# Performance work log

Hardware: AMD Instinct MI355X
Metric: run time of the kernel (lower is better)

Reference implementation:

```python
import jax, jax.numpy as jnp
import numpy as np

T = 2048          # tokens (flattened batch*seq, vLLM style)
HID = 2048        # hidden_size
NH = 16           # num_heads
D_NOPE = 128
D_ROPE = 64
D_QK = D_NOPE + D_ROPE   # 192
D_V = 128
Q_LORA = 1536
KV_LORA = 512
THETA = 10000.0
EPS = 1e-6
SCALING = D_QK ** -0.5


def _rmsnorm(x, g):
    return x * jax.lax.rsqrt(jnp.mean(x * x, axis=-1, keepdims=True) + EPS) * g


def _rope(pos, x):
    # interleaved (is_neox_style=False) rotary embedding
    d = x.shape[-1]
    inv = 1.0 / (THETA ** (jnp.arange(0, d, 2, dtype=jnp.float32) / d))
    f = pos.astype(jnp.float32)[:, None] * inv          # [T, d/2]
    cos, sin = jnp.cos(f), jnp.sin(f)
    for _ in range(x.ndim - 2):                          # broadcast over heads
        cos, sin = cos[:, None], sin[:, None]
    x1, x2 = x[..., 0::2], x[..., 1::2]
    o1 = x1 * cos - x2 * sin
    o2 = x1 * sin + x2 * cos
    return jnp.stack([o1, o2], axis=-1).reshape(x.shape)


def setup_inputs() -> dict:
    key = jax.random.key(0)
    ks = jax.random.split(key, 6)
    s = 0.02
    return {
        "hidden_states": jax.random.normal(ks[0], (T, HID), jnp.float32),
        "positions": jnp.arange(T, dtype=jnp.int32),
        "w_qkv_a": jax.random.normal(ks[1], (HID, Q_LORA + KV_LORA + D_ROPE), jnp.float32) * s,
        "g_q": jnp.ones((Q_LORA,), jnp.float32),
        "w_q_b": jax.random.normal(ks[2], (Q_LORA, NH * D_QK), jnp.float32) * s,
        "g_kv": jnp.ones((KV_LORA,), jnp.float32),
        "w_kv_b": jax.random.normal(ks[3], (KV_LORA, NH * (D_NOPE + D_V)), jnp.float32) * s,
        "w_o": jax.random.normal(ks[4], (NH * D_V, HID), jnp.float32) * s,
    }


def reference(hidden_states, positions, w_qkv_a, g_q, w_q_b, g_kv, w_kv_b, w_o):
    # fused low-rank a-projection: [T, q_lora + kv_lora + rope]
    qkv_a = hidden_states @ w_qkv_a
    q_lat = qkv_a[:, :Q_LORA]
    kv_lat = qkv_a[:, Q_LORA:Q_LORA + KV_LORA]
    k_pe = qkv_a[:, Q_LORA + KV_LORA:]                   # [T, rope]

    # query path: rmsnorm -> b-projection -> [T, H, d_qk]
    q = (_rmsnorm(q_lat, g_q) @ w_q_b).reshape(T, NH, D_QK)
    q_nope, q_pe = q[..., :D_NOPE], q[..., D_NOPE:]

    # kv path: rmsnorm -> b-projection -> [T, H, nope + v]
    kv = (_rmsnorm(kv_lat, g_kv) @ w_kv_b).reshape(T, NH, D_NOPE + D_V)
    k_nope, v = kv[..., :D_NOPE], kv[..., D_NOPE:]

    q_pe = _rope(positions, q_pe)                        # [T, H, rope]
    k_pe = _rope(positions, k_pe)                        # [T, rope] shared MQA rope key

    qf = jnp.concatenate([q_nope, q_pe], axis=-1)        # [T, H, d_qk]
    kf = jnp.concatenate([k_nope, jnp.broadcast_to(k_pe[:, None, :], (T, NH, D_ROPE))], axis=-1)

    scores = jnp.einsum("thd,shd->hts", qf, kf) * SCALING   # [H, T, T]
    mask = jnp.tril(jnp.ones((T, T), dtype=bool))
    scores = jnp.where(mask, scores, jnp.finfo(scores.dtype).min)
    probs = jax.nn.softmax(scores, axis=-1)
    out = jnp.einsum("hts,shd->thd", probs, v)           # [T, H, d_v]
    return out.reshape(T, NH * D_V) @ w_o                # [T, hidden]
```

## Files before the change

### kernel.cpp

```cpp
#include <hip/hip_runtime.h>
#include <hip/hip_bf16.h>
#include <math.h>

typedef __bf16 bf16_t;
typedef __bf16 bf16x8 __attribute__((ext_vector_type(8)));
typedef float floatx4 __attribute__((ext_vector_type(4)));
typedef int intx4 __attribute__((ext_vector_type(4)));

#define T_TOK 2048
#define HID 2048
#define NH 16
#define D_NOPE 128
#define D_ROPE 64
#define D_QK 192
#define D_V 128
#define Q_LORA 1536
#define KV_LORA 512
#define QKV_N 2112
#define QKV_NPAD 2176
#define SCALING 0.07216878364870323f
#define LOG2E 1.442695041f
#define EXP_C1 (SCALING * LOG2E)
#define EXP_C2 (12.0f * LOG2E)

#define MFMA_BF16(a, b, c) __builtin_amdgcn_mfma_f32_16x16x32_bf16(a, b, c, 0, 0, 0)

__device__ __forceinline__ void gload16(const void* g, void* l) {
    __builtin_amdgcn_global_load_lds(
        (const __attribute__((address_space(1))) unsigned int*)g,
        (__attribute__((address_space(3))) unsigned int*)l, 16, 0, 0);
}

template <int MODE>
__device__ __forceinline__ void gemm_body(
    const bf16_t* __restrict__ A, const bf16_t* __restrict__ Bt,
    float* __restrict__ Cf, bf16_t* __restrict__ Cb,
    bf16_t* __restrict__ kfull, bf16_t* __restrict__ vT,
    float* __restrict__ sqq, float* __restrict__ sqkv,
    int N, int K, int Ast, int Bst, int m0, int n0, bf16_t* S)
{
    bf16_t* As = S;
    bf16_t* Bs = S + 16384;
    const int tid = threadIdx.x;
    const int lane = tid & 63;
    const int w = tid >> 6;
    const int wm = w >> 1, wn = w & 1;
    const int l15 = lane & 15, quad = lane >> 4;
    const int ckey = (l15 >> 1) & 3;

    floatx4 acc[4][4] = {};

#define GSTAGE(db_, k0_)                                                                 \
    do {                                                                                 \
        _Pragma("unroll")                                                                \
        for (int it = 0; it < 4; ++it) {                                                 \
            int slot = it * 256 + tid;                                                   \
            int kk2 = slot >> 9;                                                         \
            int r = (slot >> 2) & 127;                                                   \
            int c = slot & 3;                                                            \
            int cs = c ^ ((r >> 1) & 3);                                                 \
            gload16((const char*)(A + (size_t)(m0 + r) * Ast + (k0_) + kk2 * 32 + cs * 8),\
                    (char*)(As + (size_t)(db_)*8192) + slot * 16);                       \
            gload16((const char*)(Bt + (size_t)(n0 + r) * Bst + (k0_) + kk2 * 32 + cs * 8),\
                    (char*)(Bs + (size_t)(db_)*8192) + slot * 16);                       \
        }                                                                                \
    } while (0)

    GSTAGE(0, 0);
    int db = 0;
    for (int k0 = 0; k0 < K; k0 += 64) {
        __syncthreads();
        if (k0 + 64 < K) GSTAGE(db ^ 1, k0 + 64);
        const bf16_t* Ab = As + (size_t)db * 8192;
        const bf16_t* Bb = Bs + (size_t)db * 8192;
#pragma unroll
        for (int kk2 = 0; kk2 < 2; ++kk2) {
            bf16x8 af[4], bfr[4];
#pragma unroll
            for (int mi = 0; mi < 4; ++mi)
                af[mi] = *(const bf16x8*)(Ab + kk2 * 4096 +
                                          (wm * 64 + mi * 16 + l15) * 32 +
                                          (quad ^ ckey) * 8);
#pragma unroll
            for (int ni = 0; ni < 4; ++ni)
                bfr[ni] = *(const bf16x8*)(Bb + kk2 * 4096 +
                                           (wn * 64 + ni * 16 + l15) * 32 +
                                           (quad ^ ckey) * 8);
#pragma unroll
            for (int mi = 0; mi < 4; ++mi)
#pragma unroll
                for (int ni = 0; ni < 4; ++ni)
                    acc[mi][ni] = MFMA_BF16(af[mi], bfr[ni], acc[mi][ni]);
        }
        db ^= 1;
    }
#undef GSTAGE

    if (MODE == 3) {
#pragma unroll
        for (int mi = 0; mi < 4; ++mi)
#pragma unroll
            for (int ni = 0; ni < 4; ++ni)
#pragma unroll
                for (int r = 0; r < 4; ++r) {
                    int row = m0 + wm * 64 + mi * 16 + quad * 4 + r;
                    int col = n0 + wn * 64 + ni * 16 + l15;
                    Cb[(size_t)row * N + col] = (bf16_t)acc[mi][ni][r];
                }
        float* sq = (n0 + 128 <= Q_LORA) ? sqq
                  : ((n0 >= Q_LORA && n0 + 128 <= Q_LORA + KV_LORA) ? sqkv : nullptr);
        if (sq) {
#pragma unroll
            for (int mi = 0; mi < 4; ++mi)
#pragma unroll
                for (int r = 0; r < 4; ++r) {
                    float s = 0.f;
#pragma unroll
                    for (int ni = 0; ni < 4; ++ni) {
                        float v = acc[mi][ni][r]; s += v * v;
                    }
                    s += __shfl_xor(s, 1); s += __shfl_xor(s, 2);
                    s += __shfl_xor(s, 4); s += __shfl_xor(s, 8);
                    if (l15 == 0)
                        atomicAdd(&sq[m0 + wm * 64 + mi * 16 + quad * 4 + r], s);
                }
        }
        return;
    }

    if (MODE == 1) {
#pragma unroll
        for (int mi = 0; mi < 4; ++mi)
#pragma unroll
            for (int r = 0; r < 4; ++r) {
                int row = m0 + wm * 64 + mi * 16 + quad * 4 + r;
                float rq = rsqrtf(sqq[row] * (1.f / Q_LORA) + 1e-6f);
#pragma unroll
                for (int ni = 0; ni < 4; ++ni) {
                    int col = n0 + wn * 64 + ni * 16 + l15;
                    Cb[(size_t)row * N + col] = (bf16_t)(acc[mi][ni][r] * rq);
                }
            }
        return;
    }

    if (MODE == 2) {
        const int hh = n0 >> 8;
        if ((n0 & 255) == 0) {
#pragma unroll
            for (int mi = 0; mi < 4; ++mi)
#pragma unroll
                for (int r = 0; r < 4; ++r) {
                    int row = m0 + wm * 64 + mi * 16 + quad * 4 + r;
                    float rkv = rsqrtf(sqkv[row] * (1.f / KV_LORA) + 1e-6f);
#pragma unroll
                    for (int ni = 0; ni < 4; ++ni) {
                        int dd = wn * 64 + ni * 16 + l15;
                        kfull[((size_t)hh * T_TOK + row) * 192 + dd] =
                            (bf16_t)(acc[mi][ni][r] * rkv);
                    }
                }
        } else {
            __syncthreads();
            bf16_t* Tq = S;
#pragma unroll
            for (int mi = 0; mi < 4; ++mi)
#pragma unroll
                for (int r = 0; r < 4; ++r) {
                    int rloc = wm * 64 + mi * 16 + quad * 4 + r;
                    float rkv = rsqrtf(sqkv[m0 + rloc] * (1.f / KV_LORA) + 1e-6f);
#pragma unroll
                    for (int ni = 0; ni < 4; ++ni) {
                        int cloc = wn * 64 + ni * 16 + l15;
                        Tq[cloc * 136 + rloc] = (bf16_t)(acc[mi][ni][r] * rkv);
                    }
                }
            __syncthreads();
#pragma unroll
            for (int pass = 0; pass < 8; ++pass) {
                int dcol = pass * 16 + w * 4 + quad;
                bf16x8 vv = *(const bf16x8*)(Tq + dcol * 136 + l15 * 8);
                *(bf16x8*)(vT + ((size_t)hh * 128 + dcol) * T_TOK + m0 + l15 * 8) = vv;
            }
        }
        return;
    }

#pragma unroll
    for (int mi = 0; mi < 4; ++mi)
#pragma unroll
        for (int ni = 0; ni < 4; ++ni)
#pragma unroll
            for (int r = 0; r < 4; ++r) {
                int row = m0 + wm * 64 + mi * 16 + quad * 4 + r;
                int col = n0 + wn * 64 + ni * 16 + l15;
                Cf[(size_t)row * N + col] = acc[mi][ni][r];
            }
}

__global__ __launch_bounds__(256) void gemm_qkv_a(
    const bf16_t* __restrict__ hbf, const bf16_t* __restrict__ wt,
    bf16_t* __restrict__ qkv_ab, float* __restrict__ sqq, float* __restrict__ sqkv)
{
    __shared__ __align__(16) bf16_t S[4 * 8192];
    gemm_body<3>(hbf, wt, nullptr, qkv_ab, nullptr, nullptr, sqq, sqkv,
                 QKV_NPAD, HID, HID, HID, blockIdx.y * 128, blockIdx.x * 128, S);
}

__global__ __launch_bounds__(256) void gemm_dual(
    const bf16_t* __restrict__ qkv_ab, const bf16_t* __restrict__ wqb,
    bf16_t* __restrict__ qbuf, const bf16_t* __restrict__ wkvb,
    bf16_t* __restrict__ kfull, bf16_t* __restrict__ vT,
    float* __restrict__ sqq, float* __restrict__ sqkv)
{
    __shared__ __align__(16) bf16_t S[4 * 8192];
    int id = blockIdx.x;
    if (id < 384) {
        gemm_body<1>(qkv_ab, wqb, nullptr, qbuf, nullptr, nullptr, sqq, nullptr,
                     3072, Q_LORA, QKV_NPAD, Q_LORA,
                     (id / 24) * 128, (id % 24) * 128, S);
    } else {
        int i2 = id - 384;
        gemm_body<2>(qkv_ab + Q_LORA, wkvb, nullptr, nullptr, kfull, vT,
                     nullptr, sqkv,
                     4096, KV_LORA, QKV_NPAD, KV_LORA,
                     (i2 / 32) * 128, (i2 % 32) * 128, S);
    }
}

__global__ __launch_bounds__(256) void gemm_out(
    const bf16_t* __restrict__ attn_o, const bf16_t* __restrict__ wto,
    float* __restrict__ out)
{
    __shared__ __align__(16) bf16_t S[4 * 8192];
    gemm_body<0>(attn_o, wto, out, nullptr, nullptr, nullptr, nullptr, nullptr,
                 HID, HID, HID, HID, blockIdx.y * 128, blockIdx.x * 128, S);
}

__global__ void transpose_all(const float* __restrict__ w0, const float* __restrict__ w1,
                              const float* __restrict__ w2, const float* __restrict__ w3,
                              const float* __restrict__ hidden,
                              const float* __restrict__ g_q, const float* __restrict__ g_kv,
                              bf16_t* __restrict__ o0, bf16_t* __restrict__ o1,
                              bf16_t* __restrict__ o2, bf16_t* __restrict__ o3,
                              bf16_t* __restrict__ hbf, float* __restrict__ sqbuf) {
    int n0 = blockIdx.x * 32, k0 = blockIdx.y * 32;
    int tx = threadIdx.x, ty = threadIdx.y;
    if (blockIdx.z == 4) {
        if (blockIdx.x == 0 && blockIdx.y == 0) {
            int t = ty * 32 + tx;
            for (int j = t; j < 4096; j += 256) sqbuf[j] = 0.f;
        }
        if (n0 >= 2048 || k0 >= 2048) return;
        for (int i = ty; i < 32; i += 8)
            hbf[(size_t)(k0 + i) * 2048 + n0 + tx] =
                (bf16_t)hidden[(size_t)(k0 + i) * 2048 + n0 + tx];
        return;
    }
    const float* in; bf16_t* out; const float* g; int K, N;
    switch (blockIdx.z) {
        case 0: in = w0; out = o0; g = nullptr; K = 2048; N = 2112; break;
        case 1: in = w1; out = o1; g = g_q;     K = 1536; N = 3072; break;
        case 2: in = w2; out = o2; g = g_kv;    K = 512;  N = 4096; break;
        default: in = w3; out = o3; g = nullptr; K = 2048; N = 2048; break;
    }
    if (n0 >= N || k0 >= K) return;
    __shared__ float tile[32][33];
    for (int i = ty; i < 32; i += 8)
        tile[i][tx] = in[(size_t)(k0 + i) * N + n0 + tx];
    __syncthreads();
    float gk = g ? g[k0 + tx] : 1.f;
    for (int i = ty; i < 32; i += 8)
        out[(size_t)(n0 + i) * K + k0 + tx] = (bf16_t)(tile[tx][i] * gk);
}

__global__ void mid_fuse_lite(const bf16_t* __restrict__ qkv_ab,
                              const int* __restrict__ pos,
                              float2* __restrict__ ropet, bf16_t* __restrict__ kfull) {
    int t = blockIdx.x, tid = threadIdx.x;
    if (tid >= 32) return;
    int i = tid;
    double inv = pow(10000.0, -(double)(2 * i) / 64.0);
    double fd = (double)pos[t] * inv;
    float c = (float)cos(fd), s = (float)sin(fd);
    ropet[t * 32 + i] = make_float2(c, s);
    float x1 = (float)qkv_ab[(size_t)t * QKV_NPAD + Q_LORA + KV_LORA + 2 * i];
    float x2 = (float)qkv_ab[(size_t)t * QKV_NPAD + Q_LORA + KV_LORA + 2 * i + 1];
    bf16_t v0 = (bf16_t)(x1 * c - x2 * s);
    bf16_t v1 = (bf16_t)(x1 * s + x2 * c);
#pragma unroll
    for (int h = 0; h < NH; ++h) {
        kfull[((size_t)h * T_TOK + t) * 192 + 128 + 2 * i] = v0;
        kfull[((size_t)h * T_TOK + t) * 192 + 128 + 2 * i + 1] = v1;
    }
}

__global__ __launch_bounds__(256, 2) void attn_part(
    const bf16_t* __restrict__ qbuf, const bf16_t* __restrict__ kfull,
    const bf16_t* __restrict__ vT, const float2* __restrict__ ropet,
    bf16_t* __restrict__ oP0, bf16_t* __restrict__ oP1, float* __restrict__ l_part)
{
    const int id = blockIdx.x;
    const int h = id & 15;
    const int c = (id >> 4) & 3;
    const int qt = 15 - (id >> 6);
    const int q0 = qt * 128;
    const int nTile = 2 * (qt + 1);
    const int tbase = nTile >> 2, trem = nTile & 3;
    const int sz = tbase + (c < trem ? 1 : 0);
    const int sBeg = c * tbase + (c < trem ? c : trem);
    const int sEnd = sBeg + sz;
    const int unit = qt * 16 + h;
    const int tid = threadIdx.x, lane = tid & 63, w = tid >> 6;
    const int l15 = lane & 15, quad = lane >> 4;
    const int ckey = (l15 >> 1) & 3;

    __shared__ __align__(16) bf16_t kn[6 * 64 * 32];
    __shared__ __align__(16) bf16_t vt2[2 * 128 * 32];
    __shared__ __align__(16) bf16_t p_s[128 * 32];

    bf16x8 qf[2][6];
#pragma unroll
    for (int st = 0; st < 2; ++st) {
        const bf16_t* qp = qbuf + (size_t)(q0 + w * 32 + st * 16 + l15) * (NH * D_QK) +
                           h * D_QK;
#pragma unroll
        for (int kk = 0; kk < 6; ++kk)
            qf[st][kk] = *(const bf16x8*)(qp + kk * 32 + quad * 8);
    }
#pragma unroll
    for (int st = 0; st < 2; ++st) {
        int t = q0 + w * 32 + st * 16 + l15;
#pragma unroll
        for (int kk = 4; kk < 6; ++kk)
#pragma unroll
            for (int p = 0; p < 4; ++p) {
                float2 cs = ropet[t * 32 + (kk - 4) * 16 + quad * 4 + p];
                float x1 = (float)qf[st][kk][2 * p], x2 = (float)qf[st][kk][2 * p + 1];
                qf[st][kk][2 * p] = (bf16_t)(x1 * cs.x - x2 * cs.y);
                qf[st][kk][2 * p + 1] = (bf16_t)(x1 * cs.y + x2 * cs.x);
            }
    }

    bf16x8 ones;
#pragma unroll
    for (int j = 0; j < 8; ++j) ones[j] = (bf16_t)1.0f;

    floatx4 o[2][8] = {};
    floatx4 lac[2] = {};
    intx4 vreg[4];

#define STAGE_KN(s0_)                                                                    \
    do {                                                                                 \
        _Pragma("unroll")                                                                \
        for (int it = 0; it < 6; ++it) {                                                 \
            int slot = it * 256 + tid;                                                   \
            int kk = slot >> 8, s = (slot >> 2) & 63, cc = slot & 3;                     \
            int cs = cc ^ ((s >> 1) & 3);                                                \
            gload16((const char*)(kfull + ((size_t)h * T_TOK + (s0_) + s) * 192 +        \
                                  kk * 32 + cs * 8),                                     \
                    (char*)kn + slot * 16);                                              \
        }                                                                                \
    } while (0)

#define VLOAD(s0_)                                                                       \
    do {                                                                                 \
        _Pragma("unroll")                                                                \
        for (int it = 0; it < 4; ++it) {                                                 \
            int slot = it * 256 + tid;                                                   \
            int ks = slot >> 9, d = (slot >> 2) & 127, cc = slot & 3;                    \
            vreg[it] = *(const intx4*)(vT + ((size_t)h * 128 + d) * T_TOK + (s0_) +      \
                                       ks * 32 + cc * 8);                                \
        }                                                                                \
    } while (0)

#define VWRITE()                                                                         \
    do {                                                                                 \
        _Pragma("unroll")                                                                \
        for (int it = 0; it < 4; ++it) {                                                 \
            int slot = it * 256 + tid;                                                   \
            int ks = slot >> 9, d = (slot >> 2) & 127, cc = slot & 3;                    \
            *(intx4*)((char*)vt2 +                                                       \
                      (size_t)((ks * 512 + d * 4 + (cc ^ ((d >> 1) & 3))) * 16)) =       \
                vreg[it];                                                                \
        }                                                                                \
    } while (0)

    if (sz > 0) {
        STAGE_KN(sBeg * 64);
        VLOAD(sBeg * 64);
        VWRITE();
    }

    for (int si = sBeg; si < sEnd; ++si) {
        const int s0 = si * 64;
        __syncthreads();

        floatx4 s_acc[2][4] = {};
        __builtin_amdgcn_s_setprio(1);
#pragma unroll
        for (int ni = 0; ni < 4; ++ni) {
#pragma unroll
            for (int kk = 0; kk < 6; ++kk) {
                bf16x8 b = *(const bf16x8*)(kn + kk * 2048 +
                                            (ni * 16 + l15) * 32 + (quad ^ ckey) * 8);
                s_acc[0][ni] = MFMA_BF16(qf[0][kk], b, s_acc[0][ni]);
                s_acc[1][ni] = MFMA_BF16(qf[1][kk], b, s_acc[1][ni]);
            }
        }
        __builtin_amdgcn_s_setprio(0);

        __syncthreads();
        if (si + 1 < sEnd) {
            STAGE_KN(s0 + 64);
            VLOAD(s0 + 64);
        }

        const bool diag = (si >= 2 * qt);
#pragma unroll
        for (int ks = 0; ks < 2; ++ks) {
#pragma unroll
            for (int st = 0; st < 2; ++st)
#pragma unroll
                for (int nl = 0; nl < 2; ++nl)
#pragma unroll
                    for (int r = 0; r < 4; ++r) {
                        int prow = w * 32 + st * 16 + quad * 4 + r;
                        int cloc = nl * 16 + l15;
                        float pv = exp2f(s_acc[st][ks * 2 + nl][r] * EXP_C1 - EXP_C2);
                        if (diag && (s0 + ks * 32 + cloc) > (q0 + prow)) pv = 0.f;
                        p_s[prow * 32 + ((((cloc >> 3) ^ ((prow >> 1) & 3))) << 3) +
                            (cloc & 7)] = (bf16_t)pv;
                    }
            __builtin_amdgcn_s_setprio(1);
            bf16x8 a0, a1;
            {
                int arow = w * 32 + l15;
                a0 = *(const bf16x8*)(p_s + arow * 32 +
                                      ((quad ^ ((arow >> 1) & 3)) << 3));
                arow += 16;
                a1 = *(const bf16x8*)(p_s + arow * 32 +
                                      ((quad ^ ((arow >> 1) & 3)) << 3));
            }
            lac[0] = MFMA_BF16(a0, ones, lac[0]);
            lac[1] = MFMA_BF16(a1, ones, lac[1]);
#pragma unroll
            for (int ni = 0; ni < 8; ++ni) {
                bf16x8 b = *(const bf16x8*)(vt2 + ks * 4096 +
                                            (ni * 16 + l15) * 32 + (quad ^ ckey) * 8);
                o[0][ni] = MFMA_BF16(a0, b, o[0][ni]);
                o[1][ni] = MFMA_BF16(a1, b, o[1][ni]);
            }
            __builtin_amdgcn_s_setprio(0);
        }

        __syncthreads();
        if (si + 1 < sEnd) VWRITE();
    }

    bf16_t* op = ((c < 2) ? oP0 : oP1) + (size_t)(unit * 2 + (c & 1)) * 128 * 128;
#pragma unroll
    for (int st = 0; st < 2; ++st) {
#pragma unroll
        for (int ni = 0; ni < 8; ++ni)
#pragma unroll
            for (int r = 0; r < 4; ++r) {
                int lrow = w * 32 + st * 16 + quad * 4 + r;
                op[(size_t)lrow * 128 + ni * 16 + l15] = (bf16_t)o[st][ni][r];
            }
        if (l15 == 0)
#pragma unroll
            for (int r = 0; r < 4; ++r) {
                int lrow = w * 32 + st * 16 + quad * 4 + r;
                l_part[((size_t)unit * 4 + c) * 128 + lrow] = lac[st][r];
            }
    }
#undef STAGE_KN
#undef VLOAD
#undef VWRITE
}

__global__ void attn_combine(const bf16_t* __restrict__ oP0,
                             const bf16_t* __restrict__ oP1,
                             const float* __restrict__ l_part,
                             bf16_t* __restrict__ attn_o)
{
    int idx = blockIdx.x * 256 + threadIdx.x;
    int t = idx >> 8, cg = idx & 255;
    int col = cg * 8;
    int h = col >> 7, d = col & 127;
    int qt = t >> 7, lrow = t & 127;
    size_t unit = (size_t)qt * 16 + h;
    const float* lp = l_part + unit * 4 * 128 + lrow;
    float inv = 1.f / (lp[0] + lp[128] + lp[256] + lp[384]);
    size_t r0 = ((unit * 2 + 0) * 128 + lrow) * 128 + d;
    size_t r1 = ((unit * 2 + 1) * 128 + lrow) * 128 + d;
    bf16x8 a0 = *(const bf16x8*)(oP0 + r0);
    bf16x8 a1 = *(const bf16x8*)(oP0 + r1);
    bf16x8 a2 = *(const bf16x8*)(oP1 + r0);
    bf16x8 a3 = *(const bf16x8*)(oP1 + r1);
    bf16x8 out;
#pragma unroll
    for (int j = 0; j < 8; ++j)
        out[j] = (bf16_t)(((float)a0[j] + (float)a1[j] + (float)a2[j] + (float)a3[j]) * inv);
    *(bf16x8*)(attn_o + (size_t)t * (NH * D_V) + col) = out;
}

extern "C" void kernel_launch(void* const* d_in, const int* in_sizes, int n_in,
                              void* d_out, int out_size, void* d_ws, size_t ws_size,
                              hipStream_t stream) {
    const float* hidden = (const float*)d_in[0];
    const int* positions = (const int*)d_in[1];
    const float* w_qkv_a = (const float*)d_in[2];
    const float* g_q = (const float*)d_in[3];
    const float* w_q_b = (const float*)d_in[4];
    const float* g_kv = (const float*)d_in[5];
    const float* w_kv_b = (const float*)d_in[6];
    const float* w_o = (const float*)d_in[7];
    float* out = (float*)d_out;

    char* p = (char*)d_ws;
    bf16_t* qkv_ab = (bf16_t*)p;
    bf16_t* attn_o = (bf16_t*)p;
    p += (size_t)T_TOK * QKV_NPAD * 4;
    bf16_t* hbf = (bf16_t*)p;
    p += (size_t)T_TOK * HID * 2;
    bf16_t* qbuf = (bf16_t*)p;  p += (size_t)T_TOK * NH * D_QK * 2;
    bf16_t* vtmp = (bf16_t*)p;  p += (size_t)T_TOK * NH * D_V * 2;
    bf16_t* kfull = (bf16_t*)p; p += (size_t)NH * T_TOK * 192 * 2;
    bf16_t* vT = (bf16_t*)p;    p += (size_t)NH * 128 * T_TOK * 2;
    bf16_t* wt_qkv_a = (bf16_t*)p; p += (size_t)QKV_NPAD * HID * 2;
    bf16_t* wt_q_b = (bf16_t*)p;   p += (size_t)3072 * Q_LORA * 2;
    bf16_t* wt_kv_b = (bf16_t*)p;  p += (size_t)4096 * KV_LORA * 2;
    bf16_t* wt_o = (bf16_t*)p;

    float2* ropet = (float2*)vtmp;
    float* l_part = (float*)((char*)vtmp + (1 << 20));
    float* sq_q = (float*)((char*)vtmp + (2 << 20));
    float* sq_kv = sq_q + 2048;
    bf16_t* oP0 = wt_qkv_a;
    bf16_t* oP1 = (bf16_t*)((char*)d_ws + (size_t)T_TOK * HID * 2);

    dim3 tb(32, 8);

    transpose_all<<<dim3(128, 64, 5), tb, 0, stream>>>(
        w_qkv_a, w_q_b, w_kv_b, w_o, hidden, g_q, g_kv,
        wt_qkv_a, wt_q_b, wt_kv_b, wt_o, hbf, sq_q);

    gemm_qkv_a<<<dim3(QKV_NPAD / 128, T_TOK / 128), 256, 0, stream>>>(
        hbf, wt_qkv_a, qkv_ab, sq_q, sq_kv);

    mid_fuse_lite<<<T_TOK, 64, 0, stream>>>(qkv_ab, positions, ropet, kfull);

    gemm_dual<<<896, 256, 0, stream>>>(qkv_ab, wt_q_b, qbuf, wt_kv_b, kfull, vT,
                                       sq_q, sq_kv);

    attn_part<<<1024, 256, 0, stream>>>(qbuf, kfull, vT, ropet, oP0, oP1, l_part);
    attn_combine<<<(T_TOK * 256) / 256, 256, 0, stream>>>(oP0, oP1, l_part, attn_o);

    gemm_out<<<dim3(HID / 128, T_TOK / 128), 256, 0, stream>>>(attn_o, wt_o, out);
}
```

Before: 301.2 us.

## Overlap weight transposes with QKV-A GEMM and fold rope into dual GEMM

```diff
diff --git a/kernel.cpp b/kernel.cpp
--- a/kernel.cpp
+++ b/kernel.cpp
@@ -198,88 +198,94 @@
             }
 }
 
-__global__ __launch_bounds__(256) void gemm_qkv_a(
+__global__ void prep(const float* __restrict__ w0, const float* __restrict__ hidden,
+                     bf16_t* __restrict__ o0, bf16_t* __restrict__ hbf,
+                     float* __restrict__ sqbuf) {
+    int n0 = blockIdx.x * 32, k0 = blockIdx.y * 32;
+    int tx = threadIdx.x, ty = threadIdx.y;
+    if (blockIdx.z == 1) {
+        if (blockIdx.x == 0 && blockIdx.y == 0) {
+            int t = ty * 32 + tx;
+            for (int j = t; j < 4096; j += 256) sqbuf[j] = 0.f;
+        }
+        if (n0 >= 2048) return;
+        for (int i = ty; i < 32; i += 8)
+            hbf[(size_t)(k0 + i) * 2048 + n0 + tx] =
+                (bf16_t)hidden[(size_t)(k0 + i) * 2048 + n0 + tx];
+        return;
+    }
+    if (n0 >= 2112) return;
+    __shared__ float tile[32][33];
+    for (int i = ty; i < 32; i += 8)
+        tile[i][tx] = w0[(size_t)(k0 + i) * 2112 + n0 + tx];
+    __syncthreads();
+    for (int i = ty; i < 32; i += 8)
+        o0[(size_t)(n0 + i) * 2048 + k0 + tx] = (bf16_t)tile[tx][i];
+}
+
+__global__ __launch_bounds__(256) void gemm_qkv_a_fused(
     const bf16_t* __restrict__ hbf, const bf16_t* __restrict__ wt,
-    bf16_t* __restrict__ qkv_ab, float* __restrict__ sqq, float* __restrict__ sqkv)
+    bf16_t* __restrict__ qkv_ab, float* __restrict__ sqq, float* __restrict__ sqkv,
+    const float* __restrict__ w1, const float* __restrict__ w2,
+    const float* __restrict__ w3,
+    const float* __restrict__ g_q, const float* __restrict__ g_kv,
+    bf16_t* __restrict__ o1, bf16_t* __restrict__ o2, bf16_t* __restrict__ o3)
 {
     __shared__ __align__(16) bf16_t S[4 * 8192];
-    gemm_body<3>(hbf, wt, nullptr, qkv_ab, nullptr, nullptr, sqq, sqkv,
-                 QKV_NPAD, HID, HID, HID, blockIdx.y * 128, blockIdx.x * 128, S);
-}
-
-__global__ __launch_bounds__(256) void gemm_dual(
+    const int id = blockIdx.x;
+    if (id < 272) {
+        gemm_body<3>(hbf, wt, nullptr, qkv_ab, nullptr, nullptr, sqq, sqkv,
+                     QKV_NPAD, HID, HID, HID, (id / 17) * 128, (id % 17) * 128, S);
+        return;
+    }
+    int e = id - 272;
+    const float* in; bf16_t* outp; const float* g; int K, N, by, bxg;
+    if (e < 288)      { in = w1; outp = o1; g = g_q;  K = 1536; N = 3072; by = e / 6; bxg = e % 6; }
+    else if (e < 416) { e -= 288; in = w2; outp = o2; g = g_kv; K = 512;  N = 4096; by = e / 8; bxg = e % 8; }
+    else              { e -= 416; in = w3; outp = o3; g = nullptr; K = 2048; N = 2048; by = e / 4; bxg = e % 4; }
+    const int tid = threadIdx.x;
+    const int tx = tid & 31, ty = tid >> 5;
+    float* tile = (float*)S;
+    const int k0 = by * 32;
+    const float gk = g ? g[k0 + tx] : 1.f;
+#pragma unroll 1
+    for (int t = 0; t < 16; ++t) {
+        int n0 = (bxg * 16 + t) * 32;
+        for (int i = ty; i < 32; i += 8)
+            tile[i * 33 + tx] = in[(size_t)(k0 + i) * N + n0 + tx];
+        __syncthreads();
+        for (int i = ty; i < 32; i += 8)
+            outp[(size_t)(n0 + i) * K + k0 + tx] = (bf16_t)(tile[tx * 33 + i] * gk);
+        __syncthreads();
+    }
+}
+
+__global__ __launch_bounds__(256) void gemm_dual_fused(
     const bf16_t* __restrict__ qkv_ab, const bf16_t* __restrict__ wqb,
     bf16_t* __restrict__ qbuf, const bf16_t* __restrict__ wkvb,
     bf16_t* __restrict__ kfull, bf16_t* __restrict__ vT,
-    float* __restrict__ sqq, float* __restrict__ sqkv)
+    float* __restrict__ sqq, float* __restrict__ sqkv,
+    const int* __restrict__ pos, float2* __restrict__ ropet)
 {
     __shared__ __align__(16) bf16_t S[4 * 8192];
-    int id = blockIdx.x;
+    const int id = blockIdx.x;
     if (id < 384) {
         gemm_body<1>(qkv_ab, wqb, nullptr, qbuf, nullptr, nullptr, sqq, nullptr,
                      3072, Q_LORA, QKV_NPAD, Q_LORA,
                      (id / 24) * 128, (id % 24) * 128, S);
-    } else {
+        return;
+    }
+    if (id < 896) {
         int i2 = id - 384;
         gemm_body<2>(qkv_ab + Q_LORA, wkvb, nullptr, nullptr, kfull, vT,
                      nullptr, sqkv,
                      4096, KV_LORA, QKV_NPAD, KV_LORA,
                      (i2 / 32) * 128, (i2 % 32) * 128, S);
-    }
-}
-
-__global__ __launch_bounds__(256) void gemm_out(
-    const bf16_t* __restrict__ attn_o, const bf16_t* __restrict__ wto,
-    float* __restrict__ out)
-{
-    __shared__ __align__(16) bf16_t S[4 * 8192];
-    gemm_body<0>(attn_o, wto, out, nullptr, nullptr, nullptr, nullptr, nullptr,
-                 HID, HID, HID, HID, blockIdx.y * 128, blockIdx.x * 128, S);
-}
-
-__global__ void transpose_all(const float* __restrict__ w0, const float* __restrict__ w1,
-                              const float* __restrict__ w2, const float* __restrict__ w3,
-                              const float* __restrict__ hidden,
-                              const float* __restrict__ g_q, const float* __restrict__ g_kv,
-                              bf16_t* __restrict__ o0, bf16_t* __restrict__ o1,
-                              bf16_t* __restrict__ o2, bf16_t* __restrict__ o3,
-                              bf16_t* __restrict__ hbf, float* __restrict__ sqbuf) {
-    int n0 = blockIdx.x * 32, k0 = blockIdx.y * 32;
-    int tx = threadIdx.x, ty = threadIdx.y;
-    if (blockIdx.z == 4) {
-        if (blockIdx.x == 0 && blockIdx.y == 0) {
-            int t = ty * 32 + tx;
-            for (int j = t; j < 4096; j += 256) sqbuf[j] = 0.f;
-        }
-        if (n0 >= 2048 || k0 >= 2048) return;
-        for (int i = ty; i < 32; i += 8)
-            hbf[(size_t)(k0 + i) * 2048 + n0 + tx] =
-                (bf16_t)hidden[(size_t)(k0 + i) * 2048 + n0 + tx];
-        return;
-    }
-    const float* in; bf16_t* out; const float* g; int K, N;
-    switch (blockIdx.z) {
-        case 0: in = w0; out = o0; g = nullptr; K = 2048; N = 2112; break;
-        case 1: in = w1; out = o1; g = g_q;     K = 1536; N = 3072; break;
-        case 2: in = w2; out = o2; g = g_kv;    K = 512;  N = 4096; break;
-        default: in = w3; out = o3; g = nullptr; K = 2048; N = 2048; break;
-    }
-    if (n0 >= N || k0 >= K) return;
-    __shared__ float tile[32][33];
-    for (int i = ty; i < 32; i += 8)
-        tile[i][tx] = in[(size_t)(k0 + i) * N + n0 + tx];
-    __syncthreads();
-    float gk = g ? g[k0 + tx] : 1.f;
-    for (int i = ty; i < 32; i += 8)
-        out[(size_t)(n0 + i) * K + k0 + tx] = (bf16_t)(tile[tx][i] * gk);
-}
-
-__global__ void mid_fuse_lite(const bf16_t* __restrict__ qkv_ab,
-                              const int* __restrict__ pos,
-                              float2* __restrict__ ropet, bf16_t* __restrict__ kfull) {
-    int t = blockIdx.x, tid = threadIdx.x;
-    if (tid >= 32) return;
-    int i = tid;
+        return;
+    }
+    int e = id - 896;
+    int t = e * 8 + (threadIdx.x >> 5);
+    int i = threadIdx.x & 31;
     double inv = pow(10000.0, -(double)(2 * i) / 64.0);
     double fd = (double)pos[t] * inv;
     float c = (float)cos(fd), s = (float)sin(fd);
@@ -293,6 +299,15 @@
         kfull[((size_t)h * T_TOK + t) * 192 + 128 + 2 * i] = v0;
         kfull[((size_t)h * T_TOK + t) * 192 + 128 + 2 * i + 1] = v1;
     }
+}
+
+__global__ __launch_bounds__(256) void gemm_out(
+    const bf16_t* __restrict__ attn_o, const bf16_t* __restrict__ wto,
+    float* __restrict__ out)
+{
+    __shared__ __align__(16) bf16_t S[4 * 8192];
+    gemm_body<0>(attn_o, wto, out, nullptr, nullptr, nullptr, nullptr, nullptr,
+                 HID, HID, HID, HID, blockIdx.y * 128, blockIdx.x * 128, S);
 }
 
 __global__ __launch_bounds__(256, 2) void attn_part(
@@ -543,17 +558,14 @@
 
     dim3 tb(32, 8);
 
-    transpose_all<<<dim3(128, 64, 5), tb, 0, stream>>>(
-        w_qkv_a, w_q_b, w_kv_b, w_o, hidden, g_q, g_kv,
-        wt_qkv_a, wt_q_b, wt_kv_b, wt_o, hbf, sq_q);
-
-    gemm_qkv_a<<<dim3(QKV_NPAD / 128, T_TOK / 128), 256, 0, stream>>>(
-        hbf, wt_qkv_a, qkv_ab, sq_q, sq_kv);
-
-    mid_fuse_lite<<<T_TOK, 64, 0, stream>>>(qkv_ab, positions, ropet, kfull);
-
-    gemm_dual<<<896, 256, 0, stream>>>(qkv_ab, wt_q_b, qbuf, wt_kv_b, kfull, vT,
-                                       sq_q, sq_kv);
+    prep<<<dim3(66, 64, 2), tb, 0, stream>>>(w_qkv_a, hidden, wt_qkv_a, hbf, sq_q);
+
+    gemm_qkv_a_fused<<<944, 256, 0, stream>>>(
+        hbf, wt_qkv_a, qkv_ab, sq_q, sq_kv,
+        w_q_b, w_kv_b, w_o, g_q, g_kv, wt_q_b, wt_kv_b, wt_o);
+
+    gemm_dual_fused<<<1152, 256, 0, stream>>>(
+        qkv_ab, wt_q_b, qbuf, wt_kv_b, kfull, vT, sq_q, sq_kv, positions, ropet);
 
     attn_part<<<1024, 256, 0, stream>>>(qbuf, kfull, vT, ropet, oP0, oP1, l_part);
     attn_combine<<<(T_TOK * 256) / 256, 256, 0, stream>>>(oP0, oP1, l_part, attn_o);
```

New measurement: 318.5 us. 1.06x slower.
